# Kernel tuning notes

Measured on AMD Instinct MI355X. Metric: run time of the kernel, lower is better.

The kernel has to match this reference:

```python
import jax, jax.numpy as jnp
import numpy as np
import math

B, N, K, NN = 16, 2048, 20, 8
IN_C, OUT_C = 64, 64
IN_CX = IN_C // 2          # in_c_x = in_c // 2 since in_c > 3
MAP = 32                   # map_size
GROUP = 4
NF = (IN_C + IN_CX) * 2    # 192 channels after repeat/relative concat


def setup_inputs() -> dict:
    key = jax.random.key(0)
    ks = jax.random.split(key, 10)
    stdv = 1.0 / math.sqrt(9.0)
    A = jax.random.uniform(ks[2], (3, 3), jnp.float32, -stdv, stdv) + 2.0 * jnp.eye(3, dtype=jnp.float32)
    return {
        "x": jax.random.normal(ks[0], (B, 3, N), jnp.float32),
        "feature": jax.random.normal(ks[1], (B, IN_C, N), jnp.float32),
        "A": A,
        "Bf": jax.random.normal(ks[3], (7, MAP), jnp.float32),
        "kernels": jax.random.normal(ks[4], (3, NN), jnp.float32),
        "one_padding": jnp.zeros((K, NN), jnp.float32).at[0, 0].set(1.0),
        "W_mlp": jax.random.normal(ks[5], (IN_CX, 2 * MAP), jnp.float32) / np.sqrt(2 * MAP).astype(np.float32),
        "b_mlp": jnp.zeros((IN_CX,), jnp.float32),
        "W1": jax.random.normal(ks[6], (OUT_C, NF), jnp.float32) / np.sqrt(NF).astype(np.float32),
        "b1": jnp.zeros((OUT_C,), jnp.float32),
        "gamma": jnp.ones((OUT_C,), jnp.float32),
        "beta": jnp.zeros((OUT_C,), jnp.float32),
        "W_out": jax.random.normal(ks[7], (OUT_C, IN_C), jnp.float32) / np.sqrt(IN_C).astype(np.float32),
    }


def knn_idx(pts, k):
    # pts: [B,N,3] -> indices of k nearest neighbors (incl. self) [B,N,k]
    sq = jnp.sum(pts * pts, axis=-1)
    d = sq[:, :, None] - 2.0 * jnp.einsum('bnd,bmd->bnm', pts, pts) + sq[:, None, :]
    _, idx = jax.lax.top_k(-d, k)
    return idx


def topkmax(p):
    # Reconstructed neighbor routing: softmax over the K-neighbor axis, then
    # zero out below-average entries (sparse 'top-k' selection).
    p = jax.nn.softmax(p, axis=2)
    return jnp.where(p > 1.0 / p.shape[2], p, 0.0)


def reference(x, feature, A, Bf, kernels, one_padding, W_mlp, b_mlp, W1, b1, gamma, beta, W_out):
    pts = jnp.transpose(x, (0, 2, 1))                      # [B,N,3]
    idx = knn_idx(pts, K)                                  # [B,N,K] int
    gather = jax.vmap(lambda p, i: p[i])                   # per-batch gather

    x_neighs = gather(pts, idx)                            # [B,N,K,3]
    x_rep = x_neighs[:, :, 0:1, :]
    x_rel = x_neighs - x_rep
    x_dis = jnp.linalg.norm(x_rel, axis=-1, keepdims=True)
    x_feats = jnp.concatenate([jnp.broadcast_to(x_rep, x_neighs.shape), x_rel, x_dis], axis=-1)  # [B,N,K,7]
    mn, mx = x_feats.min(), x_feats.max()
    x_feats = (2.0 * math.pi) * (x_feats - mn / (mx - mn))  # exact precedence as source
    x_feats = x_feats @ Bf                                  # [B,N,K,MAP]
    x_feats = jnp.concatenate([jnp.sin(x_feats), jnp.cos(x_feats)], axis=-1)  # [B,N,K,2*MAP]
    x_mlp = jnp.einsum('bnkc,oc->bnok', x_feats, W_mlp) + b_mlp[None, None, :, None]  # [B,N,IN_CX,K]

    perm = jnp.einsum('bnkd,de->bnke', x_rel, ((A + A.T) * 0.5) @ kernels) + one_padding  # [B,N,K,NN]
    perm = topkmax(perm)
    perm = perm / (jnp.sum(perm, axis=2, keepdims=True) + 1e-6)

    featN = jnp.transpose(feature, (0, 2, 1))               # [B,N,C]
    f_neigh = jnp.transpose(gather(featN, idx), (0, 1, 3, 2))  # [B,N,C,K]
    feats = jnp.concatenate([f_neigh, x_mlp], axis=2)       # [B,N,C+IN_CX,K]
    f_rep = jnp.broadcast_to(feats[:, :, :, 0:1], feats.shape)
    feats = jnp.concatenate([f_rep, feats - f_rep], axis=2)  # [B,N,NF,K]

    # group channel shuffle (num_feat > 3 + in_c_x holds)
    feats = feats.reshape(B, N, GROUP, NF // GROUP, K).transpose(0, 1, 3, 2, 4).reshape(B, N, NF, K)
    agg = jnp.einsum('bnck,bnkm->bncm', feats, perm)         # [B,N,NF,NN]
    agg = jnp.transpose(agg, (0, 2, 1, 3))                   # [B,NF,N,NN]

    h = jnp.einsum('bcnm,oc->bonm', agg, W1) + b1[None, :, None, None]
    h = jax.nn.gelu(jnp.max(h, axis=-1), approximate=False)  # [B,OUT_C,N]
    h = h + jnp.einsum('bcn,oc->bon', feature, W_out)

    # BatchNorm1d (training-mode batch stats, biased var, eps=1e-5)
    mu = jnp.mean(h, axis=(0, 2), keepdims=True)
    var = jnp.var(h, axis=(0, 2), keepdims=True)
    return gamma[None, :, None] * (h - mu) / jnp.sqrt(var + 1e-5) + beta[None, :, None]
```

## Files before the change

### kernel.cpp

```cpp
#include <hip/hip_runtime.h>
#include <math.h>

typedef __attribute__((ext_vector_type(8))) short short8v;
typedef __attribute__((ext_vector_type(4))) float float4v;

static __device__ __forceinline__ unsigned short f2bf(float f) {
  union { float f; unsigned int u; } v; v.f = f;
  unsigned int r = v.u + 0x7fffu + ((v.u >> 16) & 1u);
  return (unsigned short)(r >> 16);
}
static __device__ __forceinline__ float bf2f(unsigned short h) {
  union { unsigned int u; float f; } v; v.u = ((unsigned int)h) << 16;
  return v.f;
}
static __device__ __forceinline__ void wave_fence() {
  asm volatile("s_waitcnt lgkmcnt(0)" ::: "memory");
}

__global__ __launch_bounds__(512) void k_knn(const float* __restrict__ x,
                                             float* __restrict__ rec,
                                             int*   __restrict__ idxArr,
                                             float* __restrict__ mmPart) {
  __shared__ float px[2048], py[2048], pz[2048];
  __shared__ unsigned long long listK[8][64];
  __shared__ float wmn[8], wmx[8];

  const int b = blockIdx.y;
  const int t = threadIdx.x;
  const float* xb = x + (size_t)b * 3 * 2048;
  for (int i = t; i < 2048; i += 512) {
    px[i] = xb[i];
    py[i] = xb[2048 + i];
    pz[i] = xb[4096 + i];
  }
  __syncthreads();

  const int w = t >> 6, lane = t & 63;
  const int n = blockIdx.x * 8 + w;
  const float sx = px[n], sy = py[n], sz = pz[n];

  float lmin = 1e30f;
  for (int j = lane; j < 2048; j += 64) {
    float dx = px[j] - sx, dy = py[j] - sy, dz = pz[j] - sz;
    float d = fmaf(dx, dx, fmaf(dy, dy, dz * dz));
    lmin = fminf(lmin, d);
  }
  unsigned k32 = __float_as_uint(lmin);
  #pragma unroll
  for (int kk = 2; kk <= 64; kk <<= 1) {
    #pragma unroll
    for (int jj = kk >> 1; jj > 0; jj >>= 1) {
      unsigned o = __shfl_xor(k32, jj);
      bool keepMin = (((lane & jj) == 0) == ((lane & kk) == 0));
      unsigned mn = k32 < o ? k32 : o;
      unsigned mx = k32 < o ? o : k32;
      k32 = keepMin ? mn : mx;
    }
  }
  const float T = __uint_as_float(__shfl(k32, 19));

  int base = 0;
  for (int j = lane; j < 2048; j += 64) {
    float dx = px[j] - sx, dy = py[j] - sy, dz = pz[j] - sz;
    float d = fmaf(dx, dx, fmaf(dy, dy, dz * dz));
    bool hit = (d <= T);
    unsigned long long mask = __ballot(hit);
    if (hit) {
      int slot = base + __popcll(mask & ((1ull << lane) - 1ull));
      if (slot < 64)
        listK[w][slot] = (((unsigned long long)__float_as_uint(d)) << 32) | (unsigned)j;
    }
    base += __popcll(mask);
  }
  const int M = base;

  float myD = 0.f; int myJ = 0;
  if (M > 64) {
    float lastD = -1.f; int lastJ = -1;
    for (int r = 0; r < 20; ++r) {
      float bd = 1e30f; int bj = 0x7fffffff;
      for (int j = lane; j < 2048; j += 64) {
        float dx = px[j] - sx, dy = py[j] - sy, dz = pz[j] - sz;
        float d = fmaf(dx, dx, fmaf(dy, dy, dz * dz));
        bool valid = (d > lastD) || (d == lastD && j > lastJ);
        if (valid && (d < bd || (d == bd && j < bj))) { bd = d; bj = j; }
      }
      for (int s = 1; s < 64; s <<= 1) {
        float od = __shfl_xor(bd, s); int oj = __shfl_xor(bj, s);
        if (od < bd || (od == bd && oj < bj)) { bd = od; bj = oj; }
      }
      if (lane == r) { myD = bd; myJ = bj; }
      lastD = bd; lastJ = bj;
    }
  } else {
    wave_fence();
    unsigned long long key = (lane < M) ? listK[w][lane] : 0xFFFFFFFFFFFFFFFFull;
    #pragma unroll
    for (int kk = 2; kk <= 64; kk <<= 1) {
      #pragma unroll
      for (int jj = kk >> 1; jj > 0; jj >>= 1) {
        unsigned long long o = __shfl_xor(key, jj);
        bool keepMin = (((lane & jj) == 0) == ((lane & kk) == 0));
        unsigned long long mn = key < o ? key : o;
        unsigned long long mx = key < o ? o : key;
        key = keepMin ? mn : mx;
      }
    }
    myD = __uint_as_float((unsigned)(key >> 32));
    myJ = (int)(unsigned)(key & 0xFFFFFFFFu);
  }

  float row_mn = 1e30f, row_mx = -1e30f;
  const size_t row = (size_t)b * 2048 + n;
  if (lane < 20) {
    int j = myJ;
    idxArr[row * 20 + lane] = j;
    float rx = px[j] - sx, ry = py[j] - sy, rz = pz[j] - sz;
    float dis = sqrtf(myD);
    float* rp = rec + row * 88;
    rp[4 + lane]  = dis;
    rp[24 + lane] = rx;
    rp[44 + lane] = ry;
    rp[64 + lane] = rz;
    row_mn = fminf(fminf(rx, ry), fminf(rz, dis));
    row_mx = fmaxf(fmaxf(rx, ry), fmaxf(rz, dis));
    if (lane == 0) {
      rp[0] = sx; rp[1] = sy; rp[2] = sz; rp[3] = 0.f;
      row_mn = fminf(row_mn, fminf(fminf(sx, sy), sz));
      row_mx = fmaxf(row_mx, fmaxf(fmaxf(sx, sy), sz));
    }
  }
  for (int s = 1; s < 64; s <<= 1) {
    row_mn = fminf(row_mn, __shfl_xor(row_mn, s));
    row_mx = fmaxf(row_mx, __shfl_xor(row_mx, s));
  }
  if (lane == 0) { wmn[w] = row_mn; wmx[w] = row_mx; }
  __syncthreads();
  if (t == 0) {
    float mn = wmn[0], mx = wmx[0];
    #pragma unroll
    for (int i = 1; i < 8; ++i) { mn = fminf(mn, wmn[i]); mx = fmaxf(mx, wmx[i]); }
    int bid = blockIdx.y * 256 + blockIdx.x;
    mmPart[bid * 2]     = mn;
    mmPart[bid * 2 + 1] = mx;
  }
}

__global__ __launch_bounds__(256) void k_prep(const float* __restrict__ A,
                                              const float* __restrict__ kern,
                                              const float* __restrict__ W1,
                                              const float* __restrict__ Wmlp,
                                              const float* __restrict__ Wout,
                                              const float* __restrict__ mmPart,
                                              float* __restrict__ scal,
                                              unsigned short* __restrict__ W1Bg,
                                              unsigned short* __restrict__ WmBg,
                                              float* __restrict__ WoutT) {
  __shared__ float smn[256], smx[256];
  const int t = threadIdx.x;
  float mn = 1e30f, mx = -1e30f;
  for (int i = t; i < 4096; i += 256) {
    mn = fminf(mn, mmPart[i * 2]);
    mx = fmaxf(mx, mmPart[i * 2 + 1]);
  }
  smn[t] = mn; smx[t] = mx;
  __syncthreads();
  for (int s = 128; s > 0; s >>= 1) {
    if (t < s) { smn[t] = fminf(smn[t], smn[t + s]); smx[t] = fmaxf(smx[t], smx[t + s]); }
    __syncthreads();
  }
  if (t == 0) scal[0] = smn[0] / (smx[0] - smn[0]);
  if (t < 24) {
    int d = t >> 3, e = t & 7;
    float s = 0.f;
    for (int d2 = 0; d2 < 3; ++d2)
      s += 0.5f * (A[d * 3 + d2] + A[d2 * 3 + d]) * kern[d2 * 8 + e];
    scal[1 + t] = s;
  }
  for (int i = t; i < 12288; i += 256) {
    int o = i / 192, u = i % 192;
    int g = u / 48, r = u % 48;
    W1Bg[i] = f2bf(W1[o * 192 + r * 4 + g]);
  }
  for (int i = t; i < 2048; i += 256) WmBg[i] = f2bf(Wmlp[i]);
  for (int i = t; i < 4096; i += 256) {
    int c = i >> 6, o = i & 63;
    WoutT[c * 64 + o] = Wout[o * 64 + c];
  }
}

__global__ __launch_bounds__(256) void k_transpose(const float* __restrict__ f,
                                                   float* __restrict__ fN) {
  __shared__ float tile[64][65];
  const int b = blockIdx.y, n0 = blockIdx.x * 64, t = threadIdx.x;
  const float* fb = f + (size_t)b * 64 * 2048;
  for (int i = t; i < 4096; i += 256) {
    int c = i >> 6, nl = i & 63;
    tile[c][nl] = fb[c * 2048 + n0 + nl];
  }
  __syncthreads();
  float* out = fN + ((size_t)b * 2048 + n0) * 64;
  for (int i = t; i < 4096; i += 256) {
    int nl = i >> 6, c = i & 63;
    out[nl * 64 + c] = tile[c][nl];
  }
}

struct SMem {
  unsigned short WmB[32 * 80];
  unsigned short aggB[32 * 200];
  union {
    unsigned short ffb[4][32 * 80];
    float hB[32 * 68];
  } u;
  unsigned short xmLb[4][32 * 22];
  float recL[4][96];
  float permL[4][160];
  float f0L[4][64];
  float colsumL[4][8];
  int   idxL[4][20];
};

__global__ __launch_bounds__(256, 3) void k_main(const float* __restrict__ rec,
    const int* __restrict__ idxArr, const float* __restrict__ featN,
    const float* __restrict__ scal, const unsigned short* __restrict__ W1Bg,
    const unsigned short* __restrict__ WmBg, const float* __restrict__ WoutT,
    const float* __restrict__ Bf, const float* __restrict__ onePad,
    const float* __restrict__ bmlp, const float* __restrict__ b1,
    float* __restrict__ hT) {
  __shared__ __align__(16) SMem sm;
  const int t = threadIdx.x;
  const int pt = t >> 6, lane = t & 63;
  const int row = blockIdx.x * 4 + pt;
  const int b = row >> 11;

  for (int i = t; i < 2048; i += 256)
    sm.WmB[(i >> 6) * 80 + (i & 63)] = WmBg[i];

  if (lane < 20) sm.idxL[pt][lane] = idxArr[(size_t)row * 20 + lane];
  sm.recL[pt][lane] = rec[(size_t)row * 88 + lane];
  if (lane < 24) sm.recL[pt][64 + lane] = rec[(size_t)row * 88 + 64 + lane];

  {
    short8v z = {0, 0, 0, 0, 0, 0, 0, 0};
    *(short8v*)&sm.u.ffb[pt][(20 + (lane >> 3)) * 80 + (lane & 7) * 8] = z;
    if (lane < 32)
      *(short8v*)&sm.u.ffb[pt][(28 + (lane >> 3)) * 80 + (lane & 7) * 8] = z;
  }

  const int m31 = lane & 31;
  float bf_[7];
  #pragma unroll
  for (int d = 0; d < 7; ++d) bf_[d] = Bf[d * 32 + m31];
  const float c0 = scal[0];
  const int e7 = lane & 7;
  const float M0 = scal[1 + e7], M1 = scal[9 + e7], M2 = scal[17 + e7];
  const float bm0 = bmlp[lane & 15], bm1 = bmlp[16 + (lane & 15)];

  __syncthreads();

  {
    const float rpx = sm.recL[pt][0] - c0, rpy = sm.recL[pt][1] - c0, rpz = sm.recL[pt][2] - c0;
    const float basev = rpx * bf_[0] + rpy * bf_[1] + rpz * bf_[2];
    const int khalf = lane >> 5;
    #pragma unroll
    for (int it = 0; it < 10; ++it) {
      int k = khalf + 2 * it;
      float dis = sm.recL[pt][4 + k] - c0;
      float rx  = sm.recL[pt][24 + k] - c0;
      float ry  = sm.recL[pt][44 + k] - c0;
      float rz  = sm.recL[pt][64 + k] - c0;
      float s = basev + rx * bf_[3] + ry * bf_[4] + rz * bf_[5] + dis * bf_[6];
      float th = 6.283185307179586f * s;
      float sv, cv; __sincosf(th, &sv, &cv);
      sm.u.ffb[pt][k * 80 + m31]      = f2bf(sv);
      sm.u.ffb[pt][k * 80 + 32 + m31] = f2bf(cv);
    }
  }

  #pragma unroll
  for (int it = 0; it < 3; ++it) {
    int i = lane + 64 * it;
    if (i < 160) {
      int k = i >> 3;
      float v = sm.recL[pt][24 + k] * M0 + sm.recL[pt][44 + k] * M1
              + sm.recL[pt][64 + k] * M2 + onePad[k * 8 + e7];
      sm.permL[pt][k * 8 + e7] = v;
    }
  }
  wave_fence();

  if (lane < 8) {
    float mx = -1e30f;
    #pragma unroll
    for (int k = 0; k < 20; ++k) mx = fmaxf(mx, sm.permL[pt][k * 8 + lane]);
    float s1 = 0.f;
    #pragma unroll
    for (int k = 0; k < 20; ++k) s1 += __expf(sm.permL[pt][k * 8 + lane] - mx);
    float inv = 1.f / s1, s2 = 0.f;
    #pragma unroll
    for (int k = 0; k < 20; ++k) {
      float q = __expf(sm.permL[pt][k * 8 + lane] - mx) * inv;
      if (q > 0.05f) s2 += q;
    }
    float inv2 = 1.f / (s2 + 1e-6f);
    #pragma unroll
    for (int k = 0; k < 20; ++k) {
      float q = __expf(sm.permL[pt][k * 8 + lane] - mx) * inv;
      q = (q > 0.05f) ? q : 0.f;
      sm.permL[pt][k * 8 + lane] = q * inv2;
    }
    sm.colsumL[pt][lane] = s2 * inv2;
  }
  wave_fence();

  const int fr = lane & 15, fg = lane >> 4;
  {
    float4v acc[2][2];
    acc[0][0] = float4v{bm0, bm0, bm0, bm0};
    acc[0][1] = float4v{bm1, bm1, bm1, bm1};
    acc[1][0] = float4v{bm0, bm0, bm0, bm0};
    acc[1][1] = float4v{bm1, bm1, bm1, bm1};
    #pragma unroll
    for (int ks = 0; ks < 2; ++ks) {
      short8v a0 = *(const short8v*)&sm.u.ffb[pt][fr * 80 + ks * 32 + fg * 8];
      short8v a1 = *(const short8v*)&sm.u.ffb[pt][(16 + fr) * 80 + ks * 32 + fg * 8];
      short8v b0 = *(const short8v*)&sm.WmB[fr * 80 + ks * 32 + fg * 8];
      short8v b1v = *(const short8v*)&sm.WmB[(16 + fr) * 80 + ks * 32 + fg * 8];
      acc[0][0] = __builtin_amdgcn_mfma_f32_16x16x32_bf16(a0, b0,  acc[0][0], 0, 0, 0);
      acc[0][1] = __builtin_amdgcn_mfma_f32_16x16x32_bf16(a0, b1v, acc[0][1], 0, 0, 0);
      acc[1][0] = __builtin_amdgcn_mfma_f32_16x16x32_bf16(a1, b0,  acc[1][0], 0, 0, 0);
      acc[1][1] = __builtin_amdgcn_mfma_f32_16x16x32_bf16(a1, b1v, acc[1][1], 0, 0, 0);
    }
    #pragma unroll
    for (int mt = 0; mt < 2; ++mt)
      #pragma unroll
      for (int nt = 0; nt < 2; ++nt)
        #pragma unroll
        for (int rg = 0; rg < 4; ++rg) {
          int kk = mt * 16 + 4 * fg + rg;
          if (kk < 20)
            sm.xmLb[pt][(nt * 16 + fr) * 22 + kk] = f2bf(acc[mt][nt][rg]);
        }
  }
  wave_fence();

  float cs[8];
  {
    float4v c01 = *(const float4v*)&sm.colsumL[pt][0];
    float4v c23 = *(const float4v*)&sm.colsumL[pt][4];
    cs[0] = c01[0]; cs[1] = c01[1]; cs[2] = c01[2]; cs[3] = c01[3];
    cs[4] = c23[0]; cs[5] = c23[1]; cs[6] = c23[2]; cs[7] = c23[3];
  }
  {
    float acc[8];
    #pragma unroll
    for (int e = 0; e < 8; ++e) acc[e] = 0.f;
    float f0 = 0.f;
    const float* fNb = featN + (((size_t)b << 11) * 64);
    #pragma unroll
    for (int k = 0; k < 20; ++k) {
      int j = sm.idxL[pt][k];
      float v = fNb[j * 64 + lane];
      if (k == 0) f0 = v;
      float4v p0 = *(const float4v*)&sm.permL[pt][k * 8];
      float4v p1 = *(const float4v*)&sm.permL[pt][k * 8 + 4];
      acc[0] = fmaf(v, p0[0], acc[0]); acc[1] = fmaf(v, p0[1], acc[1]);
      acc[2] = fmaf(v, p0[2], acc[2]); acc[3] = fmaf(v, p0[3], acc[3]);
      acc[4] = fmaf(v, p1[0], acc[4]); acc[5] = fmaf(v, p1[1], acc[5]);
      acc[6] = fmaf(v, p1[2], acc[6]); acc[7] = fmaf(v, p1[3], acc[7]);
    }
    sm.f0L[pt][lane] = f0;
    #pragma unroll
    for (int e = 0; e < 8; ++e) {
      float repv = f0 * cs[e];
      sm.aggB[(pt * 8 + e) * 200 + lane]      = f2bf(repv);
      sm.aggB[(pt * 8 + e) * 200 + 96 + lane] = f2bf(acc[e] - repv);
    }
  }
  {
    const int o2 = lane & 31, hf = lane >> 5;
    float accX[8];
    #pragma unroll
    for (int e = 0; e < 8; ++e) accX[e] = 0.f;
    #pragma unroll
    for (int kk = 0; kk < 10; ++kk) {
      int k = hf * 10 + kk;
      float xv = bf2f(sm.xmLb[pt][o2 * 22 + k]);
      float4v p0 = *(const float4v*)&sm.permL[pt][k * 8];
      float4v p1 = *(const float4v*)&sm.permL[pt][k * 8 + 4];
      accX[0] = fmaf(xv, p0[0], accX[0]); accX[1] = fmaf(xv, p0[1], accX[1]);
      accX[2] = fmaf(xv, p0[2], accX[2]); accX[3] = fmaf(xv, p0[3], accX[3]);
      accX[4] = fmaf(xv, p1[0], accX[4]); accX[5] = fmaf(xv, p1[1], accX[5]);
      accX[6] = fmaf(xv, p1[2], accX[6]); accX[7] = fmaf(xv, p1[3], accX[7]);
    }
    #pragma unroll
    for (int e = 0; e < 8; ++e) accX[e] += __shfl_xor(accX[e], 32);
    float xm0 = bf2f(sm.xmLb[pt][o2 * 22]);
    if (hf == 0) {
      #pragma unroll
      for (int e = 0; e < 8; ++e)
        sm.aggB[(pt * 8 + e) * 200 + 64 + o2] = f2bf(xm0 * cs[e]);
    } else {
      #pragma unroll
      for (int e = 0; e < 8; ++e)
        sm.aggB[(pt * 8 + e) * 200 + 160 + o2] = f2bf(accX[e] - xm0 * cs[e]);
    }
  }
  __syncthreads();

  {
    const int mt = pt & 1, ntb = (pt >> 1) * 2;
    float4v h0 = float4v{0.f, 0.f, 0.f, 0.f};
    float4v h1 = float4v{0.f, 0.f, 0.f, 0.f};
    const unsigned short* w1p0 = W1Bg + ((ntb * 16 + fr) * 192);
    const unsigned short* w1p1 = W1Bg + (((ntb + 1) * 16 + fr) * 192);
    #pragma unroll
    for (int ks = 0; ks < 6; ++ks) {
      short8v a  = *(const short8v*)&sm.aggB[(mt * 16 + fr) * 200 + ks * 32 + fg * 8];
      short8v b0 = *(const short8v*)(w1p0 + ks * 32 + fg * 8);
      short8v b1v = *(const short8v*)(w1p1 + ks * 32 + fg * 8);
      h0 = __builtin_amdgcn_mfma_f32_16x16x32_bf16(a, b0,  h0, 0, 0, 0);
      h1 = __builtin_amdgcn_mfma_f32_16x16x32_bf16(a, b1v, h1, 0, 0, 0);
    }
    #pragma unroll
    for (int rg = 0; rg < 4; ++rg) {
      int m = mt * 16 + 4 * fg + rg;
      sm.u.hB[m * 68 + ntb * 16 + fr]       = h0[rg];
      sm.u.hB[m * 68 + (ntb + 1) * 16 + fr] = h1[rg];
    }
  }
  __syncthreads();

  {
    const int o = lane;
    float hm = sm.u.hB[(pt * 8) * 68 + o];
    #pragma unroll
    for (int e = 1; e < 8; ++e) hm = fmaxf(hm, sm.u.hB[(pt * 8 + e) * 68 + o]);
    hm += b1[o];
    float g = 0.5f * hm * (1.f + erff(hm * 0.7071067811865476f));
    float res = 0.f;
    #pragma unroll 8
    for (int c = 0; c < 64; ++c)
      res = fmaf(WoutT[c * 64 + o], sm.f0L[pt][c], res);
    hT[(size_t)row * 64 + o] = g + res;
  }
}

__global__ __launch_bounds__(256) void k_bnstat(const float* __restrict__ hT,
                                                float* __restrict__ part) {
  const int bk = blockIdx.x;
  const int t = threadIdx.x;
  const int o = t & 63, rg = t >> 6;
  float s = 0.f, s2 = 0.f;
  for (int r = bk * 512 + rg; r < (bk + 1) * 512; r += 4) {
    float v = hT[(size_t)r * 64 + o];
    s += v;
    s2 = fmaf(v, v, s2);
  }
  __shared__ float ls[256], ls2[256];
  ls[t] = s; ls2[t] = s2;
  __syncthreads();
  if (t < 64) {
    float a  = ls[t] + ls[t + 64] + ls[t + 128] + ls[t + 192];
    float a2 = ls2[t] + ls2[t + 64] + ls2[t + 128] + ls2[t + 192];
    part[(bk * 64 + t) * 2]     = a;
    part[(bk * 64 + t) * 2 + 1] = a2;
  }
}

__global__ void k_bnfinal(const float* __restrict__ part, float* __restrict__ stats) {
  const int t = threadIdx.x;
  if (t < 64) {
    float s = 0.f, s2 = 0.f;
    for (int bk = 0; bk < 64; ++bk) {
      s  += part[(bk * 64 + t) * 2];
      s2 += part[(bk * 64 + t) * 2 + 1];
    }
    float mu  = s * (1.f / 32768.f);
    float var = s2 * (1.f / 32768.f) - mu * mu;
    stats[t * 2]     = mu;
    stats[t * 2 + 1] = 1.f / sqrtf(var + 1e-5f);
  }
}

__global__ __launch_bounds__(256) void k_bnapply(const float* __restrict__ hT,
                                                 const float* __restrict__ stats,
                                                 const float* __restrict__ gamma,
                                                 const float* __restrict__ beta,
                                                 float* __restrict__ out) {
  __shared__ float tile[64][65];
  __shared__ float sMu[64], sRs[64], sGa[64], sBe[64];
  const int t = threadIdx.x;
  const int r0 = blockIdx.x * 64;
  if (t < 64) {
    sMu[t] = stats[t * 2];
    sRs[t] = stats[t * 2 + 1];
    sGa[t] = gamma[t];
    sBe[t] = beta[t];
  }
  __syncthreads();
  for (int i = t; i < 4096; i += 256) {
    int rl = i >> 6, o = i & 63;
    float v = hT[(size_t)(r0 + rl) * 64 + o];
    tile[rl][o] = fmaf((v - sMu[o]) * sRs[o], sGa[o], sBe[o]);
  }
  __syncthreads();
  const int b = r0 >> 11, n0 = r0 & 2047;
  for (int i = t; i < 4096; i += 256) {
    int o = i >> 6, nl = i & 63;
    out[((size_t)b * 64 + o) * 2048 + n0 + nl] = tile[nl][o];
  }
}

extern "C" void kernel_launch(void* const* d_in, const int* in_sizes, int n_in,
                              void* d_out, int out_size, void* d_ws, size_t ws_size,
                              hipStream_t stream) {
  const float* x       = (const float*)d_in[0];
  const float* feature = (const float*)d_in[1];
  const float* A       = (const float*)d_in[2];
  const float* Bf      = (const float*)d_in[3];
  const float* kern    = (const float*)d_in[4];
  const float* onePad  = (const float*)d_in[5];
  const float* Wmlp    = (const float*)d_in[6];
  const float* bmlp    = (const float*)d_in[7];
  const float* W1      = (const float*)d_in[8];
  const float* b1      = (const float*)d_in[9];
  const float* gamma   = (const float*)d_in[10];
  const float* beta    = (const float*)d_in[11];
  const float* Wout    = (const float*)d_in[12];

  char* ws = (char*)d_ws;
  float* rec             = (float*)(ws);
  int*   idxA            = (int*)  (ws + 11534336);
  float* featN           = (float*)(ws + 14155776);
  float* hT              = (float*)(ws + 22544384);
  unsigned short* W1Bg   = (unsigned short*)(ws + 30932992);
  unsigned short* WmBg   = (unsigned short*)(ws + 30957568);
  float* WoutT           = (float*)(ws + 30961664);
  float* mmPart          = (float*)(ws + 30978048);
  float* scal            = (float*)(ws + 31010816);
  float* bnPart          = (float*)(ws + 31011072);
  float* bnStats         = (float*)(ws + 31043840);

  k_knn<<<dim3(256, 16), 512, 0, stream>>>(x, rec, idxA, mmPart);
  k_prep<<<1, 256, 0, stream>>>(A, kern, W1, Wmlp, Wout, mmPart, scal, W1Bg, WmBg, WoutT);
  k_transpose<<<dim3(32, 16), 256, 0, stream>>>(feature, featN);
  k_main<<<8192, 256, 0, stream>>>(rec, idxA, featN, scal, W1Bg, WmBg, WoutT,
                                   Bf, onePad, bmlp, b1, hT);
  k_bnstat<<<64, 256, 0, stream>>>(hT, bnPart);
  k_bnfinal<<<1, 64, 0, stream>>>(bnPart, bnStats);
  k_bnapply<<<512, 256, 0, stream>>>(hT, bnStats, gamma, beta, (float*)d_out);
}
```

Baseline: 270.2 us.

## Slim k_main shared memory, prefetch neighbor gathers, reduce max in registers

Restructures k_main to shrink LDS. It drops the staged WmB copy and reads WmBg from global, trims padded ffb rows, and removes the hB staging buffer by taking the per-point max over the 8 outputs directly from MFMA accumulators with a shuffle. It also issues the 20 neighbor-feature gathers early into registers via shuffled indices, removes one block barrier, and computes the residual with vectorized Wout row reads instead of a prep-time transpose. Launch bounds rise to 4 blocks per CU to raise occupancy, at the cost of more register pressure from the 20-element gather array.

```diff
diff --git a/kernel.cpp b/kernel.cpp
--- a/kernel.cpp
+++ b/kernel.cpp
@@ -150,12 +150,10 @@
                                               const float* __restrict__ kern,
                                               const float* __restrict__ W1,
                                               const float* __restrict__ Wmlp,
-                                              const float* __restrict__ Wout,
                                               const float* __restrict__ mmPart,
                                               float* __restrict__ scal,
                                               unsigned short* __restrict__ W1Bg,
-                                              unsigned short* __restrict__ WmBg,
-                                              float* __restrict__ WoutT) {
+                                              unsigned short* __restrict__ WmBg) {
   __shared__ float smn[256], smx[256];
   const int t = threadIdx.x;
   float mn = 1e30f, mx = -1e30f;
@@ -183,10 +181,6 @@
     W1Bg[i] = f2bf(W1[o * 192 + r * 4 + g]);
   }
   for (int i = t; i < 2048; i += 256) WmBg[i] = f2bf(Wmlp[i]);
-  for (int i = t; i < 4096; i += 256) {
-    int c = i >> 6, o = i & 63;
-    WoutT[c * 64 + o] = Wout[o * 64 + c];
-  }
 }
 
 __global__ __launch_bounds__(256) void k_transpose(const float* __restrict__ f,
@@ -206,46 +200,40 @@
   }
 }
 
-struct SMem {
-  unsigned short WmB[32 * 80];
-  unsigned short aggB[32 * 200];
-  union {
-    unsigned short ffb[4][32 * 80];
-    float hB[32 * 68];
-  } u;
-  unsigned short xmLb[4][32 * 22];
-  float recL[4][96];
-  float permL[4][160];
-  float f0L[4][64];
-  float colsumL[4][8];
-  int   idxL[4][20];
-};
-
-__global__ __launch_bounds__(256, 3) void k_main(const float* __restrict__ rec,
+__global__ __launch_bounds__(256, 4) void k_main(const float* __restrict__ rec,
     const int* __restrict__ idxArr, const float* __restrict__ featN,
     const float* __restrict__ scal, const unsigned short* __restrict__ W1Bg,
-    const unsigned short* __restrict__ WmBg, const float* __restrict__ WoutT,
-    const float* __restrict__ Bf, const float* __restrict__ onePad,
-    const float* __restrict__ bmlp, const float* __restrict__ b1,
+    const unsigned short* __restrict__ WmBg, const float* __restrict__ Bf,
+    const float* __restrict__ onePad, const float* __restrict__ bmlp,
+    const float* __restrict__ b1, const float* __restrict__ Wout,
     float* __restrict__ hT) {
-  __shared__ __align__(16) SMem sm;
+  __shared__ __align__(16) unsigned short ffb[4][20 * 72];
+  __shared__ __align__(16) unsigned short aggB[32 * 200];
+  __shared__ __align__(16) unsigned short xmLb[4][32 * 22];
+  __shared__ float permL[4][160];
+  __shared__ float recL[4][96];
+  __shared__ float selfFL[4][64];
+  __shared__ float f0L[4][64];
+  __shared__ float colsumL[4][8];
+
   const int t = threadIdx.x;
   const int pt = t >> 6, lane = t & 63;
   const int row = blockIdx.x * 4 + pt;
   const int b = row >> 11;
 
-  for (int i = t; i < 2048; i += 256)
-    sm.WmB[(i >> 6) * 80 + (i & 63)] = WmBg[i];
-
-  if (lane < 20) sm.idxL[pt][lane] = idxArr[(size_t)row * 20 + lane];
-  sm.recL[pt][lane] = rec[(size_t)row * 88 + lane];
-  if (lane < 24) sm.recL[pt][64 + lane] = rec[(size_t)row * 88 + 64 + lane];
-
-  {
-    short8v z = {0, 0, 0, 0, 0, 0, 0, 0};
-    *(short8v*)&sm.u.ffb[pt][(20 + (lane >> 3)) * 80 + (lane & 7) * 8] = z;
-    if (lane < 32)
-      *(short8v*)&sm.u.ffb[pt][(28 + (lane >> 3)) * 80 + (lane & 7) * 8] = z;
+  recL[pt][lane] = rec[(size_t)row * 88 + lane];
+  if (lane < 24) recL[pt][64 + lane] = rec[(size_t)row * 88 + 64 + lane];
+  selfFL[pt][lane] = featN[(size_t)row * 64 + lane];
+  int myidx = 0;
+  if (lane < 20) myidx = idxArr[(size_t)row * 20 + lane];
+  float gv[20];
+  {
+    const float* fNb = featN + (((size_t)b << 11) * 64);
+    #pragma unroll
+    for (int k = 0; k < 20; ++k) {
+      int j = __shfl(myidx, k);
+      gv[k] = fNb[(size_t)j * 64 + lane];
+    }
   }
 
   const int m31 = lane & 31;
@@ -256,25 +244,24 @@
   const int e7 = lane & 7;
   const float M0 = scal[1 + e7], M1 = scal[9 + e7], M2 = scal[17 + e7];
   const float bm0 = bmlp[lane & 15], bm1 = bmlp[16 + (lane & 15)];
-
-  __syncthreads();
-
-  {
-    const float rpx = sm.recL[pt][0] - c0, rpy = sm.recL[pt][1] - c0, rpz = sm.recL[pt][2] - c0;
+  wave_fence();
+
+  {
+    const float rpx = recL[pt][0] - c0, rpy = recL[pt][1] - c0, rpz = recL[pt][2] - c0;
     const float basev = rpx * bf_[0] + rpy * bf_[1] + rpz * bf_[2];
     const int khalf = lane >> 5;
     #pragma unroll
     for (int it = 0; it < 10; ++it) {
       int k = khalf + 2 * it;
-      float dis = sm.recL[pt][4 + k] - c0;
-      float rx  = sm.recL[pt][24 + k] - c0;
-      float ry  = sm.recL[pt][44 + k] - c0;
-      float rz  = sm.recL[pt][64 + k] - c0;
+      float dis = recL[pt][4 + k] - c0;
+      float rx  = recL[pt][24 + k] - c0;
+      float ry  = recL[pt][44 + k] - c0;
+      float rz  = recL[pt][64 + k] - c0;
       float s = basev + rx * bf_[3] + ry * bf_[4] + rz * bf_[5] + dis * bf_[6];
       float th = 6.283185307179586f * s;
       float sv, cv; __sincosf(th, &sv, &cv);
-      sm.u.ffb[pt][k * 80 + m31]      = f2bf(sv);
-      sm.u.ffb[pt][k * 80 + 32 + m31] = f2bf(cv);
+      ffb[pt][k * 72 + m31]      = f2bf(sv);
+      ffb[pt][k * 72 + 32 + m31] = f2bf(cv);
     }
   }
 
@@ -283,9 +270,9 @@
     int i = lane + 64 * it;
     if (i < 160) {
       int k = i >> 3;
-      float v = sm.recL[pt][24 + k] * M0 + sm.recL[pt][44 + k] * M1
-              + sm.recL[pt][64 + k] * M2 + onePad[k * 8 + e7];
-      sm.permL[pt][k * 8 + e7] = v;
+      float v = recL[pt][24 + k] * M0 + recL[pt][44 + k] * M1
+              + recL[pt][64 + k] * M2 + onePad[k * 8 + e7];
+      permL[pt][k * 8 + e7] = v;
     }
   }
   wave_fence();
@@ -293,62 +280,65 @@
   if (lane < 8) {
     float mx = -1e30f;
     #pragma unroll
-    for (int k = 0; k < 20; ++k) mx = fmaxf(mx, sm.permL[pt][k * 8 + lane]);
+    for (int k = 0; k < 20; ++k) mx = fmaxf(mx, permL[pt][k * 8 + lane]);
     float s1 = 0.f;
     #pragma unroll
-    for (int k = 0; k < 20; ++k) s1 += __expf(sm.permL[pt][k * 8 + lane] - mx);
+    for (int k = 0; k < 20; ++k) s1 += __expf(permL[pt][k * 8 + lane] - mx);
     float inv = 1.f / s1, s2 = 0.f;
     #pragma unroll
     for (int k = 0; k < 20; ++k) {
-      float q = __expf(sm.permL[pt][k * 8 + lane] - mx) * inv;
+      float q = __expf(permL[pt][k * 8 + lane] - mx) * inv;
       if (q > 0.05f) s2 += q;
     }
     float inv2 = 1.f / (s2 + 1e-6f);
     #pragma unroll
     for (int k = 0; k < 20; ++k) {
-      float q = __expf(sm.permL[pt][k * 8 + lane] - mx) * inv;
+      float q = __expf(permL[pt][k * 8 + lane] - mx) * inv;
       q = (q > 0.05f) ? q : 0.f;
-      sm.permL[pt][k * 8 + lane] = q * inv2;
-    }
-    sm.colsumL[pt][lane] = s2 * inv2;
+      permL[pt][k * 8 + lane] = q * inv2;
+    }
+    colsumL[pt][lane] = s2 * inv2;
   }
   wave_fence();
 
   const int fr = lane & 15, fg = lane >> 4;
   {
-    float4v acc[2][2];
-    acc[0][0] = float4v{bm0, bm0, bm0, bm0};
-    acc[0][1] = float4v{bm1, bm1, bm1, bm1};
-    acc[1][0] = float4v{bm0, bm0, bm0, bm0};
-    acc[1][1] = float4v{bm1, bm1, bm1, bm1};
+    float4v acc00 = float4v{bm0, bm0, bm0, bm0};
+    float4v acc01 = float4v{bm1, bm1, bm1, bm1};
+    float4v acc10 = float4v{bm0, bm0, bm0, bm0};
+    float4v acc11 = float4v{bm1, bm1, bm1, bm1};
     #pragma unroll
     for (int ks = 0; ks < 2; ++ks) {
-      short8v a0 = *(const short8v*)&sm.u.ffb[pt][fr * 80 + ks * 32 + fg * 8];
-      short8v a1 = *(const short8v*)&sm.u.ffb[pt][(16 + fr) * 80 + ks * 32 + fg * 8];
-      short8v b0 = *(const short8v*)&sm.WmB[fr * 80 + ks * 32 + fg * 8];
-      short8v b1v = *(const short8v*)&sm.WmB[(16 + fr) * 80 + ks * 32 + fg * 8];
-      acc[0][0] = __builtin_amdgcn_mfma_f32_16x16x32_bf16(a0, b0,  acc[0][0], 0, 0, 0);
-      acc[0][1] = __builtin_amdgcn_mfma_f32_16x16x32_bf16(a0, b1v, acc[0][1], 0, 0, 0);
-      acc[1][0] = __builtin_amdgcn_mfma_f32_16x16x32_bf16(a1, b0,  acc[1][0], 0, 0, 0);
-      acc[1][1] = __builtin_amdgcn_mfma_f32_16x16x32_bf16(a1, b1v, acc[1][1], 0, 0, 0);
-    }
-    #pragma unroll
-    for (int mt = 0; mt < 2; ++mt)
+      short8v a0 = *(const short8v*)&ffb[pt][fr * 72 + ks * 32 + fg * 8];
+      short8v a1 = *(const short8v*)&ffb[pt][(4 + fr) * 72 + ks * 32 + fg * 8];
+      short8v b0 = *(const short8v*)(WmBg + fr * 64 + ks * 32 + fg * 8);
+      short8v b1v = *(const short8v*)(WmBg + (16 + fr) * 64 + ks * 32 + fg * 8);
+      acc00 = __builtin_amdgcn_mfma_f32_16x16x32_bf16(a0, b0,  acc00, 0, 0, 0);
+      acc01 = __builtin_amdgcn_mfma_f32_16x16x32_bf16(a0, b1v, acc01, 0, 0, 0);
+      acc10 = __builtin_amdgcn_mfma_f32_16x16x32_bf16(a1, b0,  acc10, 0, 0, 0);
+      acc11 = __builtin_amdgcn_mfma_f32_16x16x32_bf16(a1, b1v, acc11, 0, 0, 0);
+    }
+    #pragma unroll
+    for (int rg = 0; rg < 4; ++rg) {
+      int kk0 = 4 * fg + rg;
+      xmLb[pt][fr * 22 + kk0]        = f2bf(acc00[rg]);
+      xmLb[pt][(16 + fr) * 22 + kk0] = f2bf(acc01[rg]);
+    }
+    if (fg == 3) {
       #pragma unroll
-      for (int nt = 0; nt < 2; ++nt)
-        #pragma unroll
-        for (int rg = 0; rg < 4; ++rg) {
-          int kk = mt * 16 + 4 * fg + rg;
-          if (kk < 20)
-            sm.xmLb[pt][(nt * 16 + fr) * 22 + kk] = f2bf(acc[mt][nt][rg]);
-        }
+      for (int rg = 0; rg < 4; ++rg) {
+        int kk1 = 16 + rg;
+        xmLb[pt][fr * 22 + kk1]        = f2bf(acc10[rg]);
+        xmLb[pt][(16 + fr) * 22 + kk1] = f2bf(acc11[rg]);
+      }
+    }
   }
   wave_fence();
 
   float cs[8];
   {
-    float4v c01 = *(const float4v*)&sm.colsumL[pt][0];
-    float4v c23 = *(const float4v*)&sm.colsumL[pt][4];
+    float4v c01 = *(const float4v*)&colsumL[pt][0];
+    float4v c23 = *(const float4v*)&colsumL[pt][4];
     cs[0] = c01[0]; cs[1] = c01[1]; cs[2] = c01[2]; cs[3] = c01[3];
     cs[4] = c23[0]; cs[5] = c23[1]; cs[6] = c23[2]; cs[7] = c23[3];
   }
@@ -356,26 +346,23 @@
     float acc[8];
     #pragma unroll
     for (int e = 0; e < 8; ++e) acc[e] = 0.f;
-    float f0 = 0.f;
-    const float* fNb = featN + (((size_t)b << 11) * 64);
     #pragma unroll
     for (int k = 0; k < 20; ++k) {
-      int j = sm.idxL[pt][k];
-      float v = fNb[j * 64 + lane];
-      if (k == 0) f0 = v;
-      float4v p0 = *(const float4v*)&sm.permL[pt][k * 8];
-      float4v p1 = *(const float4v*)&sm.permL[pt][k * 8 + 4];
+      float v = gv[k];
+      float4v p0 = *(const float4v*)&permL[pt][k * 8];
+      float4v p1 = *(const float4v*)&permL[pt][k * 8 + 4];
       acc[0] = fmaf(v, p0[0], acc[0]); acc[1] = fmaf(v, p0[1], acc[1]);
       acc[2] = fmaf(v, p0[2], acc[2]); acc[3] = fmaf(v, p0[3], acc[3]);
       acc[4] = fmaf(v, p1[0], acc[4]); acc[5] = fmaf(v, p1[1], acc[5]);
       acc[6] = fmaf(v, p1[2], acc[6]); acc[7] = fmaf(v, p1[3], acc[7]);
     }
-    sm.f0L[pt][lane] = f0;
+    float f0 = gv[0];
+    f0L[pt][lane] = f0;
     #pragma unroll
     for (int e = 0; e < 8; ++e) {
       float repv = f0 * cs[e];
-      sm.aggB[(pt * 8 + e) * 200 + lane]      = f2bf(repv);
-      sm.aggB[(pt * 8 + e) * 200 + 96 + lane] = f2bf(acc[e] - repv);
+      aggB[(pt * 8 + e) * 200 + lane]      = f2bf(repv);
+      aggB[(pt * 8 + e) * 200 + 96 + lane] = f2bf(acc[e] - repv);
     }
   }
   {
@@ -386,9 +373,9 @@
     #pragma unroll
     for (int kk = 0; kk < 10; ++kk) {
       int k = hf * 10 + kk;
-      float xv = bf2f(sm.xmLb[pt][o2 * 22 + k]);
-      float4v p0 = *(const float4v*)&sm.permL[pt][k * 8];
-      float4v p1 = *(const float4v*)&sm.permL[pt][k * 8 + 4];
+      float xv = bf2f(xmLb[pt][o2 * 22 + k]);
+      float4v p0 = *(const float4v*)&permL[pt][k * 8];
+      float4v p1 = *(const float4v*)&permL[pt][k * 8 + 4];
       accX[0] = fmaf(xv, p0[0], accX[0]); accX[1] = fmaf(xv, p0[1], accX[1]);
       accX[2] = fmaf(xv, p0[2], accX[2]); accX[3] = fmaf(xv, p0[3], accX[3]);
       accX[4] = fmaf(xv, p1[0], accX[4]); accX[5] = fmaf(xv, p1[1], accX[5]);
@@ -396,55 +383,58 @@
     }
     #pragma unroll
     for (int e = 0; e < 8; ++e) accX[e] += __shfl_xor(accX[e], 32);
-    float xm0 = bf2f(sm.xmLb[pt][o2 * 22]);
+    float xm0 = bf2f(xmLb[pt][o2 * 22]);
     if (hf == 0) {
       #pragma unroll
       for (int e = 0; e < 8; ++e)
-        sm.aggB[(pt * 8 + e) * 200 + 64 + o2] = f2bf(xm0 * cs[e]);
+        aggB[(pt * 8 + e) * 200 + 64 + o2] = f2bf(xm0 * cs[e]);
     } else {
       #pragma unroll
       for (int e = 0; e < 8; ++e)
-        sm.aggB[(pt * 8 + e) * 200 + 160 + o2] = f2bf(accX[e] - xm0 * cs[e]);
-    }
-  }
-  __syncthreads();
-
-  {
-    const int mt = pt & 1, ntb = (pt >> 1) * 2;
-    float4v h0 = float4v{0.f, 0.f, 0.f, 0.f};
-    float4v h1 = float4v{0.f, 0.f, 0.f, 0.f};
+        aggB[(pt * 8 + e) * 200 + 160 + o2] = f2bf(accX[e] - xm0 * cs[e]);
+    }
+  }
+  __syncthreads();
+
+  const int mt = pt & 1, ntb = (pt >> 1) * 2;
+  float4v h0 = float4v{0.f, 0.f, 0.f, 0.f};
+  float4v h1 = float4v{0.f, 0.f, 0.f, 0.f};
+  {
+    const unsigned short* aRow = &aggB[(mt * 16 + fr) * 200];
     const unsigned short* w1p0 = W1Bg + ((ntb * 16 + fr) * 192);
     const unsigned short* w1p1 = W1Bg + (((ntb + 1) * 16 + fr) * 192);
     #pragma unroll
     for (int ks = 0; ks < 6; ++ks) {
-      short8v a  = *(const short8v*)&sm.aggB[(mt * 16 + fr) * 200 + ks * 32 + fg * 8];
+      short8v a  = *(const short8v*)(aRow + ks * 32 + fg * 8);
       short8v b0 = *(const short8v*)(w1p0 + ks * 32 + fg * 8);
       short8v b1v = *(const short8v*)(w1p1 + ks * 32 + fg * 8);
       h0 = __builtin_amdgcn_mfma_f32_16x16x32_bf16(a, b0,  h0, 0, 0, 0);
       h1 = __builtin_amdgcn_mfma_f32_16x16x32_bf16(a, b1v, h1, 0, 0, 0);
     }
-    #pragma unroll
-    for (int rg = 0; rg < 4; ++rg) {
-      int m = mt * 16 + 4 * fg + rg;
-      sm.u.hB[m * 68 + ntb * 16 + fr]       = h0[rg];
-      sm.u.hB[m * 68 + (ntb + 1) * 16 + fr] = h1[rg];
-    }
-  }
-  __syncthreads();
-
-  {
-    const int o = lane;
-    float hm = sm.u.hB[(pt * 8) * 68 + o];
-    #pragma unroll
-    for (int e = 1; e < 8; ++e) hm = fmaxf(hm, sm.u.hB[(pt * 8 + e) * 68 + o]);
-    hm += b1[o];
+  }
+
+  {
+    float m0 = fmaxf(fmaxf(h0[0], h0[1]), fmaxf(h0[2], h0[3]));
+    float m1 = fmaxf(fmaxf(h1[0], h1[1]), fmaxf(h1[2], h1[3]));
+    m0 = fmaxf(m0, __shfl_xor(m0, 16));
+    m1 = fmaxf(m1, __shfl_xor(m1, 16));
+    const int p_loc = 2 * mt + (fg >> 1);
+    const int col = (ntb + (fg & 1)) * 16 + fr;
+    float hm = ((fg & 1) ? m1 : m0) + b1[col];
     float g = 0.5f * hm * (1.f + erff(hm * 0.7071067811865476f));
     float res = 0.f;
-    #pragma unroll 8
-    for (int c = 0; c < 64; ++c)
-      res = fmaf(WoutT[c * 64 + o], sm.f0L[pt][c], res);
-    hT[(size_t)row * 64 + o] = g + res;
-  }
+    const float* wr = Wout + col * 64;
+    #pragma unroll
+    for (int c = 0; c < 64; c += 4) {
+      float4 wv = *(const float4*)(wr + c);
+      res = fmaf(wv.x, selfFL[p_loc][c],     res);
+      res = fmaf(wv.y, selfFL[p_loc][c + 1], res);
+      res = fmaf(wv.z, selfFL[p_loc][c + 2], res);
+      res = fmaf(wv.w, selfFL[p_loc][c + 3], res);
+    }
+    hT[(size_t)(blockIdx.x * 4 + p_loc) * 64 + col] = g + res;
+  }
+  (void)f0L;
 }
 
 __global__ __launch_bounds__(256) void k_bnstat(const float* __restrict__ hT,
@@ -537,17 +527,16 @@
   float* hT              = (float*)(ws + 22544384);
   unsigned short* W1Bg   = (unsigned short*)(ws + 30932992);
   unsigned short* WmBg   = (unsigned short*)(ws + 30957568);
-  float* WoutT           = (float*)(ws + 30961664);
-  float* mmPart          = (float*)(ws + 30978048);
-  float* scal            = (float*)(ws + 31010816);
-  float* bnPart          = (float*)(ws + 31011072);
-  float* bnStats         = (float*)(ws + 31043840);
+  float* mmPart          = (float*)(ws + 30961664);
+  float* scal            = (float*)(ws + 30994432);
+  float* bnPart          = (float*)(ws + 30994688);
+  float* bnStats         = (float*)(ws + 31027456);
 
   k_knn<<<dim3(256, 16), 512, 0, stream>>>(x, rec, idxA, mmPart);
-  k_prep<<<1, 256, 0, stream>>>(A, kern, W1, Wmlp, Wout, mmPart, scal, W1Bg, WmBg, WoutT);
+  k_prep<<<1, 256, 0, stream>>>(A, kern, W1, Wmlp, mmPart, scal, W1Bg, WmBg);
   k_transpose<<<dim3(32, 16), 256, 0, stream>>>(feature, featN);
-  k_main<<<8192, 256, 0, stream>>>(rec, idxA, featN, scal, W1Bg, WmBg, WoutT,
-                                   Bf, onePad, bmlp, b1, hT);
+  k_main<<<8192, 256, 0, stream>>>(rec, idxA, featN, scal, W1Bg, WmBg,
+                                   Bf, onePad, bmlp, b1, Wout, hT);
   k_bnstat<<<64, 256, 0, stream>>>(hT, bnPart);
   k_bnfinal<<<1, 64, 0, stream>>>(bnPart, bnStats);
   k_bnapply<<<512, 256, 0, stream>>>(hT, bnStats, gamma, beta, (float*)d_out);
```

Measured after the change: 288.6 us. 1.07x slower.
